# Kernel optimization log

Hardware: AMD Instinct MI355X
Metric: run time of the kernel (lower is better)

## Reference

```python
import jax, jax.numpy as jnp
import numpy as np

B, S, IN, OUT, E, K = 4, 2048, 4096, 4096, 8, 16
POOLS = E * K  # 128 rank-one pools


def setup_inputs() -> dict:
    key = jax.random.key(0)
    k1, k2, k3, k4, k5 = jax.random.split(key, 5)
    sc = 0.02
    return {
        "hidden_states": jax.random.normal(k1, (B, S, IN), jnp.float32),
        "w0": jax.random.normal(k2, (OUT, IN), jnp.float32) * sc,   # pretrained Linear weight
        "b0": jnp.zeros((OUT,), jnp.float32),                        # pretrained Linear bias
        "wr": jax.random.normal(k3, (POOLS, IN), jnp.float32) * sc,  # Router stacked v.T
        "u": jax.random.normal(k4, (OUT, POOLS), jnp.float32) * sc,  # RankOnePools.u
        "svh": jax.random.normal(k5, (POOLS, IN), jnp.float32) * sc, # RankOnePools.svh
        "top_k": 2,
    }


def reference(hidden_states, w0, b0, wr, u, svh, top_k):
    # pretrained dense path (expert_use_diff=True)
    pretrained_out = jnp.einsum('bsi,oi->bso', hidden_states, w0) + b0

    x = hidden_states.reshape(-1, hidden_states.shape[-1])  # [N, IN]

    # Router: logits over num_experts*k rank-one pools
    logits = jnp.einsum('ni,pi->np', x, wr)                  # [N, POOLS]
    vals, idx = jax.lax.top_k(logits, top_k)                 # [N, top_k]
    vals = vals / jnp.sum(vals, axis=-1, keepdims=True)      # computed but UNUSED (matches original torch code)

    # RankOnePools: gather selected rank-one factors and combine
    svh_sel = svh[idx]                                       # [N, top_k, IN]
    dot = jnp.einsum('ni,nti->nt', x, svh_sel)               # [N, top_k]
    u_sel = u.T[idx]                                         # [N, top_k, OUT]
    expert_out = jnp.einsum('nt,nto->no', dot, u_sel)        # [N, OUT]

    out = pretrained_out + expert_out.reshape(pretrained_out.shape)
    return out
```

## Files before the change

kernel.cpp:

```cpp
#include <hip/hip_runtime.h>

#define K_DIM  4096
#define N_OUT  4096
#define N_TOK  8192
#define N_POOL 128

typedef __bf16 bf16x8 __attribute__((ext_vector_type(8)));
typedef float  f32x4  __attribute__((ext_vector_type(4)));
typedef unsigned short u16x8 __attribute__((ext_vector_type(8)));

__device__ __forceinline__ unsigned short f2bf(float f) {
    union { float f; unsigned u; } v; v.f = f;
    unsigned r = v.u + 0x7fffu + ((v.u >> 16) & 1u);
    return (unsigned short)(r >> 16);
}
__device__ __forceinline__ float bf2f(unsigned short b) {
    union { unsigned u; float f; } v; v.u = ((unsigned)b) << 16;
    return v.f;
}

__global__ __launch_bounds__(256) void k_convert_w0(const float* __restrict__ w0,
                                                    unsigned short* __restrict__ w0b) {
    size_t base = ((size_t)blockIdx.x * 256 + threadIdx.x) * 8;
    float4 a = *(const float4*)(w0 + base);
    float4 b = *(const float4*)(w0 + base + 4);
    u16x8 r;
    r[0] = f2bf(a.x); r[1] = f2bf(a.y); r[2] = f2bf(a.z); r[3] = f2bf(a.w);
    r[4] = f2bf(b.x); r[5] = f2bf(b.y); r[6] = f2bf(b.z); r[7] = f2bf(b.w);
    *(u16x8*)(w0b + base) = r;
}

__global__ __launch_bounds__(256) void k_split_wr(const float* __restrict__ wr,
                                                  unsigned short* __restrict__ wrh,
                                                  unsigned short* __restrict__ wrl) {
    size_t base = ((size_t)blockIdx.x * 256 + threadIdx.x) * 4;
    float4 a = *(const float4*)(wr + base);
    ushort4 h, l;
    h.x = f2bf(a.x); h.y = f2bf(a.y); h.z = f2bf(a.z); h.w = f2bf(a.w);
    l.x = f2bf(a.x - bf2f(h.x)); l.y = f2bf(a.y - bf2f(h.y));
    l.z = f2bf(a.z - bf2f(h.z)); l.w = f2bf(a.w - bf2f(h.w));
    *(ushort4*)(wrh + base) = h;
    *(ushort4*)(wrl + base) = l;
}

__global__ __launch_bounds__(256) void k_transpose_u(const float* __restrict__ u,
                                                     float* __restrict__ uT) {
    __shared__ float t[32][65];
    const int o0 = blockIdx.x * 64, p0 = blockIdx.y * 32;
    const int tid = threadIdx.x;
#pragma unroll
    for (int it = 0; it < 8; it++) {
        int o = (tid >> 5) + it * 8;
        t[tid & 31][o] = u[(size_t)(o0 + o) * N_POOL + p0 + (tid & 31)];
    }
    __syncthreads();
#pragma unroll
    for (int it = 0; it < 8; it++) {
        int p = (tid >> 6) + it * 4;
        uT[(size_t)(p0 + p) * N_OUT + o0 + (tid & 63)] = t[p][tid & 63];
    }
}

#define RTK 64
#define TAU 0.01f

__global__ __launch_bounds__(512) void k_router(const float* __restrict__ x,
                                                const float* __restrict__ wr,
                                                const unsigned short* __restrict__ wrh,
                                                const unsigned short* __restrict__ wrl,
                                                const float* __restrict__ svh,
                                                unsigned short* __restrict__ xb,
                                                int* __restrict__ idxp,
                                                float* __restrict__ dotp) {
    __shared__ __attribute__((aligned(16))) unsigned short Ah[32 * RTK];
    __shared__ __attribute__((aligned(16))) unsigned short Al[32 * RTK];
    __shared__ __attribute__((aligned(16))) unsigned short Bh[N_POOL * RTK];
    __shared__ __attribute__((aligned(16))) unsigned short Bl[N_POOL * RTK];
    __shared__ float lg[32][N_POOL + 1];
    __shared__ float thr2[32];
    __shared__ int   flg[32];
    __shared__ int   sel[32][2];

    const int tid  = threadIdx.x;
    const int lane = tid & 63;
    const int w    = tid >> 6;
    const int wm   = w & 1;
    const int wn   = w >> 1;
    const int lrow = lane & 15, lquad = lane >> 4;
    const size_t m0 = (size_t)blockIdx.x * 32;

    const int atok  = tid >> 4;
    const int akoff = (tid & 15) * 4;
    const int aswz  = ((((tid & 15) >> 1) ^ (atok & 7)) * 8) + (tid & 1) * 4;

    const int brow = tid >> 3;

    float4 x_pf = *(const float4*)(x + (m0 + atok) * K_DIM + akoff);

    f32x4 acc[2] = {};

    for (int k0 = 0; k0 < K_DIM; k0 += RTK) {
        __syncthreads();
        {
            ushort4 h, l;
            h.x = f2bf(x_pf.x); h.y = f2bf(x_pf.y); h.z = f2bf(x_pf.z); h.w = f2bf(x_pf.w);
            l.x = f2bf(x_pf.x - bf2f(h.x)); l.y = f2bf(x_pf.y - bf2f(h.y));
            l.z = f2bf(x_pf.z - bf2f(h.z)); l.w = f2bf(x_pf.w - bf2f(h.w));
            *(ushort4*)(xb + (m0 + atok) * K_DIM + k0 + akoff) = h;
            *(ushort4*)(&Ah[atok * RTK + aswz]) = h;
            *(ushort4*)(&Al[atok * RTK + aswz]) = l;
        }
#pragma unroll
        for (int i = 0; i < 2; i++) {
            const int r = brow + i * 64;
            const int c = (tid & 7) ^ (r & 7);
            __builtin_amdgcn_global_load_lds(
                (const __attribute__((address_space(1))) void*)(wrh + (size_t)r * K_DIM + k0 + c * 8),
                (__attribute__((address_space(3))) void*)(Bh + i * 4096 + tid * 8), 16, 0, 0);
            __builtin_amdgcn_global_load_lds(
                (const __attribute__((address_space(1))) void*)(wrl + (size_t)r * K_DIM + k0 + c * 8),
                (__attribute__((address_space(3))) void*)(Bl + i * 4096 + tid * 8), 16, 0, 0);
        }
        __syncthreads();
        if (k0 + RTK < K_DIM)
            x_pf = *(const float4*)(x + (m0 + atok) * K_DIM + k0 + RTK + akoff);
#pragma unroll
        for (int ks = 0; ks < 2; ks++) {
            const int cs = ((ks * 4 + lquad) ^ (lrow & 7)) * 8;
            bf16x8 ah = *(const bf16x8*)&Ah[(wm * 16 + lrow) * RTK + cs];
            bf16x8 al = *(const bf16x8*)&Al[(wm * 16 + lrow) * RTK + cs];
#pragma unroll
            for (int nt = 0; nt < 2; nt++) {
                bf16x8 bh = *(const bf16x8*)&Bh[(wn * 32 + nt * 16 + lrow) * RTK + cs];
                bf16x8 bl = *(const bf16x8*)&Bl[(wn * 32 + nt * 16 + lrow) * RTK + cs];
                acc[nt] = __builtin_amdgcn_mfma_f32_16x16x32_bf16(ah, bh, acc[nt], 0, 0, 0);
                acc[nt] = __builtin_amdgcn_mfma_f32_16x16x32_bf16(ah, bl, acc[nt], 0, 0, 0);
                acc[nt] = __builtin_amdgcn_mfma_f32_16x16x32_bf16(al, bh, acc[nt], 0, 0, 0);
            }
        }
    }

#pragma unroll
    for (int nt = 0; nt < 2; nt++)
#pragma unroll
        for (int r = 0; r < 4; r++)
            lg[wm * 16 + lquad * 4 + r][wn * 32 + nt * 16 + lrow] = acc[nt][r];
    __syncthreads();

    if (tid < 32) {
        float v1 = -3.4e38f, v2 = -3.4e38f, v3 = -3.4e38f; int i1 = 0, i2 = 0;
        for (int p = 0; p < N_POOL; p++) {
            float v = lg[tid][p];
            if (v > v1)      { v3 = v2; v2 = v1; i2 = i1; v1 = v; i1 = p; }
            else if (v > v2) { v3 = v2; v2 = v;  i2 = p; }
            else if (v > v3) { v3 = v; }
        }
        sel[tid][0] = i1; sel[tid][1] = i2;
        thr2[tid] = v2 - TAU;
        flg[tid]  = (v2 - v3 < TAU) ? 1 : 0;
    }
    __syncthreads();

    if (w == 0) {
        for (int s = 0; s < 32; s++) {
            if (!flg[s]) continue;
            const float th = thr2[s];
            unsigned long long c0 = __ballot(lg[s][lane] >= th);
            unsigned long long c1 = __ballot(lg[s][64 + lane] >= th);
            float v1 = -3.4e38f, v2 = -3.4e38f; int i1 = 0, i2 = 0;
            const float* xr = x + (m0 + s) * K_DIM;
            for (int half = 0; half < 2; half++) {
                unsigned long long m = half ? c1 : c0;
                while (m) {
                    const int p = (half ? 64 : 0) + __ffsll(m) - 1;
                    m &= m - 1;
                    const float* wp = wr + (size_t)p * K_DIM;
                    float d = 0.f;
#pragma unroll 8
                    for (int it = 0; it < 64; it++)
                        d += xr[it * 64 + lane] * wp[it * 64 + lane];
#pragma unroll
                    for (int off = 32; off > 0; off >>= 1) d += __shfl_down(d, off);
                    d = __shfl(d, 0);
                    if (d > v1)      { v2 = v1; i2 = i1; v1 = d; i1 = p; }
                    else if (d > v2) { v2 = d; i2 = p; }
                }
            }
            if (lane == 0) { sel[s][0] = i1; sel[s][1] = i2; }
        }
    }
    __syncthreads();

    if (tid < 32) {
        idxp[(m0 + tid) * 2 + 0] = sel[tid][0];
        idxp[(m0 + tid) * 2 + 1] = sel[tid][1];
    }

    for (int s = w; s < 32; s += 8) {
        const size_t n = m0 + s;
        const int e0 = sel[s][0], e1 = sel[s][1];
        float d0 = 0.f, d1 = 0.f;
#pragma unroll
        for (int it = 0; it < 8; it++) {
            const int e = (it * 64 + lane) * 8;
            u16x8 xv = *(const u16x8*)(xb + n * K_DIM + e);
            float4 s0 = *(const float4*)(svh + (size_t)e0 * K_DIM + e);
            float4 s1 = *(const float4*)(svh + (size_t)e0 * K_DIM + e + 4);
            float4 s2 = *(const float4*)(svh + (size_t)e1 * K_DIM + e);
            float4 s3 = *(const float4*)(svh + (size_t)e1 * K_DIM + e + 4);
            float x0 = bf2f(xv[0]), x1 = bf2f(xv[1]), x2 = bf2f(xv[2]), x3 = bf2f(xv[3]);
            float x4 = bf2f(xv[4]), x5 = bf2f(xv[5]), x6 = bf2f(xv[6]), x7 = bf2f(xv[7]);
            d0 += x0*s0.x + x1*s0.y + x2*s0.z + x3*s0.w + x4*s1.x + x5*s1.y + x6*s1.z + x7*s1.w;
            d1 += x0*s2.x + x1*s2.y + x2*s2.z + x3*s2.w + x4*s3.x + x5*s3.y + x6*s3.z + x7*s3.w;
        }
#pragma unroll
        for (int off = 32; off > 0; off >>= 1) {
            d0 += __shfl_down(d0, off);
            d1 += __shfl_down(d1, off);
        }
        if (lane == 0) { dotp[n * 2 + 0] = d0; dotp[n * 2 + 1] = d1; }
    }
}

__global__ __launch_bounds__(512) void k_gemm(const unsigned short* __restrict__ xb,
                                              const unsigned short* __restrict__ w0b,
                                              const float* __restrict__ b0,
                                              const float* __restrict__ uT,
                                              const int* __restrict__ idxp,
                                              const float* __restrict__ dotp,
                                              float* __restrict__ out) {
    __shared__ __attribute__((aligned(16))) unsigned short Als[2][256 * 64];
    __shared__ __attribute__((aligned(16))) unsigned short Bls[2][256 * 64];

    const int tid  = threadIdx.x;
    const int lane = tid & 63;
    const int w    = tid >> 6;
    const int wm   = w >> 2, wn = w & 3;
    const int lrow = lane & 15, lquad = lane >> 4;

    const int lg = (blockIdx.x & 7) * 64 + (blockIdx.x >> 3);
    const size_t n0 = (size_t)(lg & 15) * 256;
    const size_t m0 = (size_t)(lg >> 4) * 256;

    const int srow   = tid >> 3;
    const int xchunk = (tid & 7) ^ (srow & 7);
    const unsigned short* ag = xb  + (m0 + srow) * K_DIM + xchunk * 8;
    const unsigned short* bg = w0b + (n0 + srow) * K_DIM + xchunk * 8;

    f32x4 acc[8][4] = {};

#define STAGE(buf, k0)                                                                        \
    {                                                                                         \
        unsigned short* al = &Als[buf][tid * 8];                                              \
        unsigned short* bl = &Bls[buf][tid * 8];                                              \
        _Pragma("unroll")                                                                     \
        for (int l = 0; l < 4; l++) {                                                         \
            __builtin_amdgcn_global_load_lds(                                                 \
                (const __attribute__((address_space(1))) void*)(ag + (size_t)l * 64 * K_DIM + (k0)), \
                (__attribute__((address_space(3))) void*)(al + l * 4096), 16, 0, 0);          \
            __builtin_amdgcn_global_load_lds(                                                 \
                (const __attribute__((address_space(1))) void*)(bg + (size_t)l * 64 * K_DIM + (k0)), \
                (__attribute__((address_space(3))) void*)(bl + l * 4096), 16, 0, 0);          \
        }                                                                                     \
    }

#define COMPUTE(buf)                                                                          \
    {                                                                                         \
        _Pragma("unroll")                                                                     \
        for (int ks = 0; ks < 2; ks++) {                                                      \
            const int cs = ((ks * 4 + lquad) ^ (lrow & 7)) * 8;                               \
            bf16x8 bfv[4];                                                                    \
            _Pragma("unroll")                                                                 \
            for (int nt = 0; nt < 4; nt++)                                                    \
                bfv[nt] = *(const bf16x8*)&Bls[buf][(wn * 64 + nt * 16 + lrow) * 64 + cs];    \
            _Pragma("unroll")                                                                 \
            for (int mt = 0; mt < 8; mt++) {                                                  \
                bf16x8 av = *(const bf16x8*)&Als[buf][(wm * 128 + mt * 16 + lrow) * 64 + cs]; \
                _Pragma("unroll")                                                             \
                for (int nt = 0; nt < 4; nt++)                                                \
                    acc[mt][nt] = __builtin_amdgcn_mfma_f32_16x16x32_bf16(av, bfv[nt], acc[mt][nt], 0, 0, 0); \
            }                                                                                 \
        }                                                                                     \
    }

    STAGE(0, 0)
    STAGE(1, 64)

    for (int t = 0; t < 63; ++t) {
        asm volatile("s_waitcnt vmcnt(8)" ::: "memory");
        __builtin_amdgcn_s_barrier();
        const int buf = t & 1;
        COMPUTE(buf)
        __builtin_amdgcn_s_barrier();
        if (t < 62) STAGE(buf, (t + 2) * 64)
    }
    asm volatile("s_waitcnt vmcnt(0)" ::: "memory");
    __builtin_amdgcn_s_barrier();
    COMPUTE(1)

#undef STAGE
#undef COMPUTE

    float b0v[4];
#pragma unroll
    for (int nt = 0; nt < 4; nt++) b0v[nt] = b0[n0 + wn * 64 + nt * 16 + lrow];
#pragma unroll
    for (int mt = 0; mt < 8; mt++) {
        const size_t rb = m0 + wm * 128 + mt * 16 + lquad * 4;
#pragma unroll
        for (int r = 0; r < 4; r++) {
            const size_t gm = rb + r;
            const int e0 = idxp[gm * 2 + 0], e1 = idxp[gm * 2 + 1];
            const float dd0 = dotp[gm * 2 + 0], dd1 = dotp[gm * 2 + 1];
#pragma unroll
            for (int nt = 0; nt < 4; nt++) {
                const size_t gn = n0 + wn * 64 + nt * 16 + lrow;
                float vv = acc[mt][nt][r] + b0v[nt]
                         + dd0 * uT[(size_t)e0 * N_OUT + gn] + dd1 * uT[(size_t)e1 * N_OUT + gn];
                out[gm * N_OUT + gn] = vv;
            }
        }
    }
}

extern "C" void kernel_launch(void* const* d_in, const int* in_sizes, int n_in,
                              void* d_out, int out_size, void* d_ws, size_t ws_size,
                              hipStream_t stream) {
    const float* x   = (const float*)d_in[0];
    const float* w0  = (const float*)d_in[1];
    const float* b0  = (const float*)d_in[2];
    const float* wr  = (const float*)d_in[3];
    const float* u   = (const float*)d_in[4];
    const float* svh = (const float*)d_in[5];
    float* out = (float*)d_out;

    char* ws = (char*)d_ws;
    unsigned short* xb  = (unsigned short*)ws;
    unsigned short* w0b = (unsigned short*)(ws + 67108864);
    int*   idxp = (int*)(ws + 100663296);
    float* dotp = (float*)(ws + 100663296 + 65536);
    float* uTp  = (float*)(ws + 100663296 + 131072);
    unsigned short* wrh = (unsigned short*)(ws + 102891520);
    unsigned short* wrl = (unsigned short*)(ws + 103940096);

    k_convert_w0<<<dim3(16777216 / (256 * 8)), dim3(256), 0, stream>>>(w0, w0b);
    k_split_wr<<<dim3(N_POOL * K_DIM / (256 * 4)), dim3(256), 0, stream>>>(wr, wrh, wrl);
    k_transpose_u<<<dim3(N_OUT / 64, N_POOL / 32), dim3(256), 0, stream>>>(u, uTp);
    k_router<<<dim3(N_TOK / 32), dim3(512), 0, stream>>>(x, wr, wrh, wrl, svh, xb, idxp, dotp);
    k_gemm<<<dim3(512), dim3(512), 0, stream>>>(xb, w0b, b0, uTp, idxp, dotp, out);
}
```

Before: 680.9 us.

## Drop split-bf16 router GEMM, prestage bf16 x and double-buffer router loads

The router logits GEMM no longer uses hi/lo bf16 splits of x and wr (three MFMAs per step); it now does a single bf16 MFMA. The wider ambiguity threshold TAU widens the fp32 re-check of near-tie top-k candidates to make up for the lost precision. x is converted to bf16 in a separate kernel, and the router loads both operands via global_load_lds into a double-buffered LDS pipeline with explicit vmcnt waits. This cuts router MFMA work and per-iteration conversion, but adds a full pass over x and relies on the fallback path to keep top-k selection exact.

Result: slower. 731.2 us (+7.4%).

```diff
diff --git a/kernel.cpp b/kernel.cpp
--- a/kernel.cpp
+++ b/kernel.cpp
@@ -8,6 +8,9 @@
 typedef __bf16 bf16x8 __attribute__((ext_vector_type(8)));
 typedef float  f32x4  __attribute__((ext_vector_type(4)));
 typedef unsigned short u16x8 __attribute__((ext_vector_type(8)));
+
+#define AS1 __attribute__((address_space(1)))
+#define AS3 __attribute__((address_space(3)))
 
 __device__ __forceinline__ unsigned short f2bf(float f) {
     union { float f; unsigned u; } v; v.f = f;
@@ -30,17 +33,26 @@
     *(u16x8*)(w0b + base) = r;
 }
 
-__global__ __launch_bounds__(256) void k_split_wr(const float* __restrict__ wr,
-                                                  unsigned short* __restrict__ wrh,
-                                                  unsigned short* __restrict__ wrl) {
-    size_t base = ((size_t)blockIdx.x * 256 + threadIdx.x) * 4;
+__global__ __launch_bounds__(256) void k_convert_x(const float* __restrict__ x,
+                                                   unsigned short* __restrict__ xh) {
+    size_t base = ((size_t)blockIdx.x * 256 + threadIdx.x) * 8;
+    float4 a = *(const float4*)(x + base);
+    float4 b = *(const float4*)(x + base + 4);
+    u16x8 r;
+    r[0] = f2bf(a.x); r[1] = f2bf(a.y); r[2] = f2bf(a.z); r[3] = f2bf(a.w);
+    r[4] = f2bf(b.x); r[5] = f2bf(b.y); r[6] = f2bf(b.z); r[7] = f2bf(b.w);
+    *(u16x8*)(xh + base) = r;
+}
+
+__global__ __launch_bounds__(256) void k_convert_wr(const float* __restrict__ wr,
+                                                    unsigned short* __restrict__ wrh) {
+    size_t base = ((size_t)blockIdx.x * 256 + threadIdx.x) * 8;
     float4 a = *(const float4*)(wr + base);
-    ushort4 h, l;
-    h.x = f2bf(a.x); h.y = f2bf(a.y); h.z = f2bf(a.z); h.w = f2bf(a.w);
-    l.x = f2bf(a.x - bf2f(h.x)); l.y = f2bf(a.y - bf2f(h.y));
-    l.z = f2bf(a.z - bf2f(h.z)); l.w = f2bf(a.w - bf2f(h.w));
-    *(ushort4*)(wrh + base) = h;
-    *(ushort4*)(wrl + base) = l;
+    float4 b = *(const float4*)(wr + base + 4);
+    u16x8 r;
+    r[0] = f2bf(a.x); r[1] = f2bf(a.y); r[2] = f2bf(a.z); r[3] = f2bf(a.w);
+    r[4] = f2bf(b.x); r[5] = f2bf(b.y); r[6] = f2bf(b.z); r[7] = f2bf(b.w);
+    *(u16x8*)(wrh + base) = r;
 }
 
 __global__ __launch_bounds__(256) void k_transpose_u(const float* __restrict__ u,
@@ -62,20 +74,17 @@
 }
 
 #define RTK 64
-#define TAU 0.01f
+#define TAU 0.06f
 
 __global__ __launch_bounds__(512) void k_router(const float* __restrict__ x,
                                                 const float* __restrict__ wr,
                                                 const unsigned short* __restrict__ wrh,
-                                                const unsigned short* __restrict__ wrl,
+                                                const unsigned short* __restrict__ xh,
                                                 const float* __restrict__ svh,
-                                                unsigned short* __restrict__ xb,
                                                 int* __restrict__ idxp,
                                                 float* __restrict__ dotp) {
-    __shared__ __attribute__((aligned(16))) unsigned short Ah[32 * RTK];
-    __shared__ __attribute__((aligned(16))) unsigned short Al[32 * RTK];
-    __shared__ __attribute__((aligned(16))) unsigned short Bh[N_POOL * RTK];
-    __shared__ __attribute__((aligned(16))) unsigned short Bl[N_POOL * RTK];
+    __shared__ __attribute__((aligned(16))) unsigned short A2[2][32 * RTK];
+    __shared__ __attribute__((aligned(16))) unsigned short B2[2][N_POOL * RTK];
     __shared__ float lg[32][N_POOL + 1];
     __shared__ float thr2[32];
     __shared__ int   flg[32];
@@ -88,57 +97,50 @@
     const int wn   = w >> 1;
     const int lrow = lane & 15, lquad = lane >> 4;
     const size_t m0 = (size_t)blockIdx.x * 32;
-
-    const int atok  = tid >> 4;
-    const int akoff = (tid & 15) * 4;
-    const int aswz  = ((((tid & 15) >> 1) ^ (atok & 7)) * 8) + (tid & 1) * 4;
-
-    const int brow = tid >> 3;
-
-    float4 x_pf = *(const float4*)(x + (m0 + atok) * K_DIM + akoff);
+    const int srow8 = lane >> 3, schunk = lane & 7;
 
     f32x4 acc[2] = {};
 
-    for (int k0 = 0; k0 < K_DIM; k0 += RTK) {
-        __syncthreads();
-        {
-            ushort4 h, l;
-            h.x = f2bf(x_pf.x); h.y = f2bf(x_pf.y); h.z = f2bf(x_pf.z); h.w = f2bf(x_pf.w);
-            l.x = f2bf(x_pf.x - bf2f(h.x)); l.y = f2bf(x_pf.y - bf2f(h.y));
-            l.z = f2bf(x_pf.z - bf2f(h.z)); l.w = f2bf(x_pf.w - bf2f(h.w));
-            *(ushort4*)(xb + (m0 + atok) * K_DIM + k0 + akoff) = h;
-            *(ushort4*)(&Ah[atok * RTK + aswz]) = h;
-            *(ushort4*)(&Al[atok * RTK + aswz]) = l;
-        }
-#pragma unroll
-        for (int i = 0; i < 2; i++) {
-            const int r = brow + i * 64;
-            const int c = (tid & 7) ^ (r & 7);
-            __builtin_amdgcn_global_load_lds(
-                (const __attribute__((address_space(1))) void*)(wrh + (size_t)r * K_DIM + k0 + c * 8),
-                (__attribute__((address_space(3))) void*)(Bh + i * 4096 + tid * 8), 16, 0, 0);
-            __builtin_amdgcn_global_load_lds(
-                (const __attribute__((address_space(1))) void*)(wrl + (size_t)r * K_DIM + k0 + c * 8),
-                (__attribute__((address_space(3))) void*)(Bl + i * 4096 + tid * 8), 16, 0, 0);
-        }
-        __syncthreads();
-        if (k0 + RTK < K_DIM)
-            x_pf = *(const float4*)(x + (m0 + atok) * K_DIM + k0 + RTK + akoff);
+#define RSTAGE(bufi, kk)                                                                         \
+    {                                                                                            \
+        if (w < 4) {                                                                             \
+            int rr = 8 * w + srow8; int cc = schunk ^ (rr & 7);                                  \
+            __builtin_amdgcn_global_load_lds(                                                    \
+                (const AS1 void*)(xh + (m0 + rr) * (size_t)K_DIM + (kk) + cc * 8),               \
+                (AS3 void*)(&A2[bufi][8 * w * RTK] + lane * 8), 16, 0, 0);                       \
+        }                                                                                        \
+        _Pragma("unroll")                                                                        \
+        for (int j = 0; j < 2; j++) {                                                            \
+            int rr = 8 * w + 64 * j + srow8; int cc = schunk ^ (rr & 7);                         \
+            __builtin_amdgcn_global_load_lds(                                                    \
+                (const AS1 void*)(wrh + (size_t)rr * K_DIM + (kk) + cc * 8),                     \
+                (AS3 void*)(&B2[bufi][(8 * w + 64 * j) * RTK] + lane * 8), 16, 0, 0);            \
+        }                                                                                        \
+    }
+
+    RSTAGE(0, 0)
+    RSTAGE(1, RTK)
+
+    for (int t = 0; t < K_DIM / RTK; ++t) {
+        if (t == 63)     asm volatile("s_waitcnt vmcnt(0)" ::: "memory");
+        else if (w < 4)  asm volatile("s_waitcnt vmcnt(3)" ::: "memory");
+        else             asm volatile("s_waitcnt vmcnt(2)" ::: "memory");
+        __builtin_amdgcn_s_barrier();
+        const int buf = t & 1;
 #pragma unroll
         for (int ks = 0; ks < 2; ks++) {
             const int cs = ((ks * 4 + lquad) ^ (lrow & 7)) * 8;
-            bf16x8 ah = *(const bf16x8*)&Ah[(wm * 16 + lrow) * RTK + cs];
-            bf16x8 al = *(const bf16x8*)&Al[(wm * 16 + lrow) * RTK + cs];
+            bf16x8 ah = *(const bf16x8*)&A2[buf][(wm * 16 + lrow) * RTK + cs];
 #pragma unroll
             for (int nt = 0; nt < 2; nt++) {
-                bf16x8 bh = *(const bf16x8*)&Bh[(wn * 32 + nt * 16 + lrow) * RTK + cs];
-                bf16x8 bl = *(const bf16x8*)&Bl[(wn * 32 + nt * 16 + lrow) * RTK + cs];
+                bf16x8 bh = *(const bf16x8*)&B2[buf][(wn * 32 + nt * 16 + lrow) * RTK + cs];
                 acc[nt] = __builtin_amdgcn_mfma_f32_16x16x32_bf16(ah, bh, acc[nt], 0, 0, 0);
-                acc[nt] = __builtin_amdgcn_mfma_f32_16x16x32_bf16(ah, bl, acc[nt], 0, 0, 0);
-                acc[nt] = __builtin_amdgcn_mfma_f32_16x16x32_bf16(al, bh, acc[nt], 0, 0, 0);
             }
         }
-    }
+        __builtin_amdgcn_s_barrier();
+        if (t < 62) RSTAGE(buf, (t + 2) * RTK)
+    }
+#undef RSTAGE
 
 #pragma unroll
     for (int nt = 0; nt < 2; nt++)
@@ -203,7 +205,7 @@
 #pragma unroll
         for (int it = 0; it < 8; it++) {
             const int e = (it * 64 + lane) * 8;
-            u16x8 xv = *(const u16x8*)(xb + n * K_DIM + e);
+            u16x8 xv = *(const u16x8*)(xh + n * K_DIM + e);
             float4 s0 = *(const float4*)(svh + (size_t)e0 * K_DIM + e);
             float4 s1 = *(const float4*)(svh + (size_t)e0 * K_DIM + e + 4);
             float4 s2 = *(const float4*)(svh + (size_t)e1 * K_DIM + e);
@@ -222,7 +224,7 @@
     }
 }
 
-__global__ __launch_bounds__(512) void k_gemm(const unsigned short* __restrict__ xb,
+__global__ __launch_bounds__(512) void k_gemm(const unsigned short* __restrict__ xh,
                                               const unsigned short* __restrict__ w0b,
                                               const float* __restrict__ b0,
                                               const float* __restrict__ uT,
@@ -238,13 +240,13 @@
     const int wm   = w >> 2, wn = w & 3;
     const int lrow = lane & 15, lquad = lane >> 4;
 
-    const int lg = (blockIdx.x & 7) * 64 + (blockIdx.x >> 3);
-    const size_t n0 = (size_t)(lg & 15) * 256;
-    const size_t m0 = (size_t)(lg >> 4) * 256;
+    const int lgid = (blockIdx.x & 7) * 64 + (blockIdx.x >> 3);
+    const size_t n0 = (size_t)(lgid & 15) * 256;
+    const size_t m0 = (size_t)(lgid >> 4) * 256;
 
     const int srow   = tid >> 3;
     const int xchunk = (tid & 7) ^ (srow & 7);
-    const unsigned short* ag = xb  + (m0 + srow) * K_DIM + xchunk * 8;
+    const unsigned short* ag = xh  + (m0 + srow) * K_DIM + xchunk * 8;
     const unsigned short* bg = w0b + (n0 + srow) * K_DIM + xchunk * 8;
 
     f32x4 acc[8][4] = {};
@@ -256,11 +258,11 @@
         _Pragma("unroll")                                                                     \
         for (int l = 0; l < 4; l++) {                                                         \
             __builtin_amdgcn_global_load_lds(                                                 \
-                (const __attribute__((address_space(1))) void*)(ag + (size_t)l * 64 * K_DIM + (k0)), \
-                (__attribute__((address_space(3))) void*)(al + l * 4096), 16, 0, 0);          \
+                (const AS1 void*)(ag + (size_t)l * 64 * K_DIM + (k0)),                        \
+                (AS3 void*)(al + l * 4096), 16, 0, 0);                                        \
             __builtin_amdgcn_global_load_lds(                                                 \
-                (const __attribute__((address_space(1))) void*)(bg + (size_t)l * 64 * K_DIM + (k0)), \
-                (__attribute__((address_space(3))) void*)(bl + l * 4096), 16, 0, 0);          \
+                (const AS1 void*)(bg + (size_t)l * 64 * K_DIM + (k0)),                        \
+                (AS3 void*)(bl + l * 4096), 16, 0, 0);                                        \
         }                                                                                     \
     }
 
@@ -335,17 +337,17 @@
     float* out = (float*)d_out;
 
     char* ws = (char*)d_ws;
-    unsigned short* xb  = (unsigned short*)ws;
+    unsigned short* xh  = (unsigned short*)ws;
     unsigned short* w0b = (unsigned short*)(ws + 67108864);
     int*   idxp = (int*)(ws + 100663296);
     float* dotp = (float*)(ws + 100663296 + 65536);
     float* uTp  = (float*)(ws + 100663296 + 131072);
     unsigned short* wrh = (unsigned short*)(ws + 102891520);
-    unsigned short* wrl = (unsigned short*)(ws + 103940096);
 
     k_convert_w0<<<dim3(16777216 / (256 * 8)), dim3(256), 0, stream>>>(w0, w0b);
-    k_split_wr<<<dim3(N_POOL * K_DIM / (256 * 4)), dim3(256), 0, stream>>>(wr, wrh, wrl);
+    k_convert_x<<<dim3(33554432 / (256 * 8)), dim3(256), 0, stream>>>(x, xh);
+    k_convert_wr<<<dim3(524288 / (256 * 8)), dim3(256), 0, stream>>>(wr, wrh);
     k_transpose_u<<<dim3(N_OUT / 64, N_POOL / 32), dim3(256), 0, stream>>>(u, uTp);
-    k_router<<<dim3(N_TOK / 32), dim3(512), 0, stream>>>(x, wr, wrh, wrl, svh, xb, idxp, dotp);
-    k_gemm<<<dim3(512), dim3(512), 0, stream>>>(xb, w0b, b0, uTp, idxp, dotp, out);
-}
+    k_router<<<dim3(N_TOK / 32), dim3(512), 0, stream>>>(x, wr, wrh, xh, svh, idxp, dotp);
+    k_gemm<<<dim3(512), dim3(512), 0, stream>>>(xh, w0b, b0, uTp, idxp, dotp, out);
+}
```
